# Kernel tuning notes

Measured on AMD Instinct MI355X. Metric: run time of the kernel, lower is better.

Reference implementation:

```python
import jax, jax.numpy as jnp
import numpy as np


def setup_inputs() -> dict:
    key = jax.random.key(0)
    ks = jax.random.split(key, 12)
    Tq, Tk, B, H = 1024, 1024, 8, 1024
    inp = {
        "inputs_q": jax.random.normal(ks[0], (Tq, B, H), jnp.float32),
        "inputs_kv": jax.random.normal(ks[1], (Tk, B, H), jnp.float32),
        "w_q": jax.random.normal(ks[2], (H, H), jnp.float32) * 0.02,
        "b_q": jnp.zeros((H,), jnp.float32),
        "w_kv": jax.random.normal(ks[3], (2 * H, H), jnp.float32) * 0.02,
        "b_kv": jnp.zeros((2 * H,), jnp.float32),
        "w_o": jax.random.normal(ks[4], (H, H), jnp.float32) * 0.02,
        "b_o": jnp.zeros((H,), jnp.float32),
        # BatchEnsemble rank-1 factors, initialized near 1
        "r_q": 1.0 + 0.05 * jax.random.normal(ks[5], (B, H), jnp.float32),
        "s_q": 1.0 + 0.05 * jax.random.normal(ks[6], (B, H), jnp.float32),
        "r_kv": 1.0 + 0.05 * jax.random.normal(ks[7], (B, H), jnp.float32),
        "s_kv": 1.0 + 0.05 * jax.random.normal(ks[8], (B, 2 * H), jnp.float32),
        "heads": 16,
    }
    return inp


def be_linear(x, w, b, r, s):
    # x: [T,B,Hin], w: [Hout,Hin], r: [B,Hin], s: [B,Hout]
    return jnp.einsum('tbh,oh->tbo', x * r, w) * s + b


def reference(inputs_q, inputs_kv, w_q, b_q, w_kv, b_kv, w_o, b_o,
              r_q, s_q, r_kv, s_kv, heads):
    Tq, B, H = inputs_q.shape
    Tk = inputs_kv.shape[0]
    hd = H // heads
    scale = hd ** -0.5

    q = be_linear(inputs_q, w_q, b_q, r_q, s_q)          # [Tq,B,H]
    kv = be_linear(inputs_kv, w_kv, b_kv, r_kv, s_kv)    # [Tk,B,2H]

    queries = q.reshape(Tq, B * heads, hd)
    kv = kv.reshape(Tk, B * heads, 2, hd)                # layout: head x {k,v} x hd
    keys = kv[:, :, 0, :]
    values = kv[:, :, 1, :]

    scores = jnp.einsum('qnd,knd->nqk', queries, keys) * scale  # [B*heads,Tq,Tk]
    probs = jax.nn.softmax(scores.astype(jnp.float32), axis=-1).astype(scores.dtype)
    # dropout_prob = 0 / eval: dropout is identity
    ctx = jnp.einsum('nqk,knd->qnd', probs, values).reshape(Tq, B, H)
    out = jnp.einsum('tbh,oh->tbo', ctx, w_o) + b_o      # [Tq,B,H]
    return out
```

## Files before the change

kernel.cpp:

```cpp
#include <hip/hip_runtime.h>
#include <stdint.h>

typedef unsigned short u16;
typedef __bf16 bf16x8 __attribute__((ext_vector_type(8)));
typedef float f32x4 __attribute__((ext_vector_type(4)));

typedef __attribute__((address_space(3))) void lds_void;
typedef const __attribute__((address_space(1))) void gbl_void;
#define GLD_LDS16(g, l) __builtin_amdgcn_global_load_lds((gbl_void*)(g), (lds_void*)(l), 16, 0, 0)

__device__ __forceinline__ u16 f2bf(float f) {
  unsigned u = __float_as_uint(f);
  u += 0x7fffu + ((u >> 16) & 1u);
  return (u16)(u >> 16);
}

__device__ __forceinline__ unsigned pk2bf(float a, float b) {
  unsigned au = __float_as_uint(a) + 0x8000u;
  unsigned bu = __float_as_uint(b) + 0x8000u;
  return __builtin_amdgcn_perm(bu, au, 0x07060302u);
}

__global__ void k_convert_all(const float* __restrict__ inq, const float* __restrict__ r_q,
                              const float* __restrict__ inkv, const float* __restrict__ r_kv,
                              const float* __restrict__ w_q, const float* __restrict__ w_kv,
                              const float* __restrict__ w_o,
                              u16* __restrict__ Xq, u16* __restrict__ Xkv,
                              u16* __restrict__ Wq, u16* __restrict__ Wkv,
                              u16* __restrict__ Wo) {
  int blk = blockIdx.x;
  const float* src; const float* r = nullptr; u16* dst; int base;
  if (blk < 8192)       { src = inq;  r = r_q;  dst = Xq;  base = 0; }
  else if (blk < 16384) { src = inkv; r = r_kv; dst = Xkv; base = 8192; }
  else if (blk < 17408) { src = w_q;  dst = Wq;  base = 16384; }
  else if (blk < 19456) { src = w_kv; dst = Wkv; base = 17408; }
  else                  { src = w_o;  dst = Wo;  base = 19456; }
  int i4 = ((blk - base) * 256 + threadIdx.x) * 4;
  float4 xv = *(const float4*)(src + i4);
  if (r) {
    int rb = ((i4 >> 10) & 7) * 1024 + (i4 & 1023);
    float4 rv = *(const float4*)(r + rb);
    xv.x *= rv.x; xv.y *= rv.y; xv.z *= rv.z; xv.w *= rv.w;
  }
  unsigned long long pk = (unsigned long long)pk2bf(xv.x, xv.y)
      | ((unsigned long long)pk2bf(xv.z, xv.w) << 32);
  *(unsigned long long*)(dst + i4) = pk;
}

template <int MODE>
__device__ __forceinline__ void gemm_tile(const u16* __restrict__ A, const u16* __restrict__ B,
                                          void* __restrict__ Cout, const float* __restrict__ s,
                                          const float* __restrict__ bias, int N, int K,
                                          float postscale, int bx, int by,
                                          u16* As, u16* Bs, int tid) {
  const int w = tid >> 6, lane = tid & 63;
  const int quad = lane >> 4, l16 = lane & 15;
  const int n0 = bx * 128, m0 = by * 128;
  const int wm = (w & 1) * 64, wn = (w >> 1) * 64;

  f32x4 acc[4][4] = {};

  int srow[2], scol[2];
#pragma unroll
  for (int i = 0; i < 2; ++i) {
    int p = (w * 2 + i) * 64 + lane;
    int row = p >> 2;
    int cb = (p & 3) ^ ((row >> 1) & 3);
    srow[i] = row; scol[i] = cb * 8;
  }
  int offA[4], offB[4];
#pragma unroll
  for (int t = 0; t < 4; ++t) {
    int ra = wm + t * 16 + l16;
    offA[t] = ra * 32 + ((quad ^ ((ra >> 1) & 3)) * 8);
    int rb = wn + t * 16 + l16;
    offB[t] = rb * 32 + ((quad ^ ((rb >> 1) & 3)) * 8);
  }

#pragma unroll
  for (int i = 0; i < 2; ++i) {
    GLD_LDS16(A + (size_t)(m0 + srow[i]) * K + scol[i], As + (w * 2 + i) * 512);
    GLD_LDS16(B + (size_t)(n0 + srow[i]) * K + scol[i], Bs + (w * 2 + i) * 512);
  }

  for (int k0 = 0; k0 < K; k0 += 32) {
    const int cur = (k0 >> 5) & 1;
    __syncthreads();
    if (k0 + 32 < K) {
#pragma unroll
      for (int i = 0; i < 2; ++i) {
        GLD_LDS16(A + (size_t)(m0 + srow[i]) * K + (k0 + 32) + scol[i],
                  As + (cur ^ 1) * 4096 + (w * 2 + i) * 512);
        GLD_LDS16(B + (size_t)(n0 + srow[i]) * K + (k0 + 32) + scol[i],
                  Bs + (cur ^ 1) * 4096 + (w * 2 + i) * 512);
      }
    }
    const u16* Ac = As + cur * 4096;
    const u16* Bc = Bs + cur * 4096;
    bf16x8 af[4], bfr[4];
#pragma unroll
    for (int mt = 0; mt < 4; ++mt) af[mt] = *(const bf16x8*)(Ac + offA[mt]);
#pragma unroll
    for (int nt = 0; nt < 4; ++nt) bfr[nt] = *(const bf16x8*)(Bc + offB[nt]);
#pragma unroll
    for (int mt = 0; mt < 4; ++mt)
#pragma unroll
      for (int nt = 0; nt < 4; ++nt)
        acc[mt][nt] = __builtin_amdgcn_mfma_f32_16x16x32_bf16(af[mt], bfr[nt], acc[mt][nt], 0, 0, 0);
  }

#pragma unroll
  for (int mt = 0; mt < 4; ++mt)
#pragma unroll
    for (int nt = 0; nt < 4; ++nt) {
      int n = n0 + wn + nt * 16 + l16;
#pragma unroll
      for (int rg = 0; rg < 4; ++rg) {
        int m = m0 + wm + mt * 16 + quad * 4 + rg;
        float v = acc[mt][nt][rg];
        if (MODE == 0) {
          v = (v * s[(m & 7) * N + n] + bias[n]) * postscale;
          ((u16*)Cout)[(size_t)m * N + n] = f2bf(v);
        } else {
          ((float*)Cout)[(size_t)m * N + n] = v + bias[n];
        }
      }
    }
}

__global__ void k_gemm_qkv(const u16* __restrict__ Xq, const u16* __restrict__ Wq,
                           u16* __restrict__ qout, const float* __restrict__ s_q,
                           const float* __restrict__ b_q, float qscale,
                           const u16* __restrict__ Xkv, const u16* __restrict__ Wkv,
                           u16* __restrict__ kvout, const float* __restrict__ s_kv,
                           const float* __restrict__ b_kv) {
  __shared__ __align__(16) u16 As[2 * 4096];
  __shared__ __align__(16) u16 Bs[2 * 4096];
  const int blk = blockIdx.x;
  const int xcd = blk & 7;
  const int slot = blk >> 3;
  const int bx = slot % 24;
  const int by = xcd * 8 + slot / 24;
  if (bx < 8)
    gemm_tile<0>(Xq, Wq, qout, s_q, b_q, 1024, 1024, qscale, bx, by, As, Bs, threadIdx.x);
  else
    gemm_tile<0>(Xkv, Wkv, kvout, s_kv, b_kv, 2048, 1024, 1.0f, bx - 8, by, As, Bs, threadIdx.x);
}

__global__ void k_gemm_o(const u16* __restrict__ A, const u16* __restrict__ B,
                         float* __restrict__ Cout, const float* __restrict__ bias) {
  __shared__ __align__(16) u16 As[2 * 4096];
  __shared__ __align__(16) u16 Bs[2 * 4096];
  const int blk = blockIdx.x;
  const int xcd = blk & 7;
  const int slot = blk >> 3;
  const int bx = slot % 8;
  const int by = xcd * 8 + slot / 8;
  gemm_tile<1>(A, B, Cout, nullptr, bias, 1024, 1024, 1.0f, bx, by, As, Bs, threadIdx.x);
}

__global__ void k_transpose_v(const u16* __restrict__ kv, u16* __restrict__ vt) {
  __shared__ __align__(16) u16 tile[64][72];
  const int tid = threadIdx.x;
  const int n = blockIdx.x >> 4;
  const int t0 = (blockIdx.x & 15) << 6;
#pragma unroll
  for (int it = 0; it < 2; ++it) {
    int r = it * 32 + (tid >> 3);
    int c = (tid & 7) << 3;
    *(uint4*)&tile[r][c] = *(const uint4*)(kv + ((size_t)(t0 + r) * 128 + n) * 128 + 64 + c);
  }
  __syncthreads();
#pragma unroll
  for (int it = 0; it < 2; ++it) {
    int d = it * 32 + (tid >> 3);
    int tc = (tid & 7) << 3;
    u16 v[8];
#pragma unroll
    for (int j = 0; j < 8; ++j) v[j] = tile[tc + j][d];
    uint4 o;
    o.x = (unsigned)v[0] | ((unsigned)v[1] << 16);
    o.y = (unsigned)v[2] | ((unsigned)v[3] << 16);
    o.z = (unsigned)v[4] | ((unsigned)v[5] << 16);
    o.w = (unsigned)v[6] | ((unsigned)v[7] << 16);
    *(uint4*)(vt + ((size_t)n * 64 + d) * 1024 + t0 + tc) = o;
  }
}

__global__ __launch_bounds__(256, 3) void k_attn(const u16* __restrict__ qb,
                                                 const u16* __restrict__ kvb,
                                                 const u16* __restrict__ vtb,
                                                 u16* __restrict__ ctx) {
  __shared__ __align__(16) u16 Ks[2][4096];
  __shared__ __align__(16) u16 Vts[2][4096];
  __shared__ __align__(16) u16 Ps[4][32 * 72];

  const int tid = threadIdx.x;
  const int w = tid >> 6, lane = tid & 63;
  const int quad = lane >> 4, l16 = lane & 15;
  const int n = blockIdx.x & 127;
  const int q0 = (blockIdx.x >> 7) << 7;
  const int qw = q0 + w * 32;

  bf16x8 bq[2][2];
#pragma unroll
  for (int g = 0; g < 2; ++g)
#pragma unroll
    for (int ks = 0; ks < 2; ++ks)
      bq[g][ks] = *(const bf16x8*)(qb + ((size_t)(qw + g * 16 + l16) * 128 + n) * 64 + ks * 32 + quad * 8);

  const bool isK = (w < 2);
  const int wv = w & 1;
  const u16* gbase[4];
  u16* lbase[4];
#pragma unroll
  for (int i = 0; i < 4; ++i) {
    int p = (wv * 4 + i) * 64 + lane;
    int r = p >> 3;
    int scb = ((p & 7) ^ (r & 7)) * 8;
    if (isK) {
      gbase[i] = kvb + ((size_t)r * 128 + n) * 128 + scb;
      lbase[i] = &Ks[0][(wv * 4 + i) * 512];
    } else {
      gbase[i] = vtb + ((size_t)n * 64 + r) * 1024 + scb;
      lbase[i] = &Vts[0][(wv * 4 + i) * 512];
    }
  }
  const size_t gstep = isK ? 16384 : 1;
  const int lstep = 4096;

  float l_i[2] = {0.f, 0.f};
  f32x4 accO[2][4] = {};
  u16* myP = Ps[w];

#pragma unroll
  for (int i = 0; i < 4; ++i) GLD_LDS16(gbase[i], lbase[i]);

#pragma unroll 1
  for (int tk0 = 0; tk0 < 1024; tk0 += 64) {
    const int cur = (tk0 >> 6) & 1;
    __syncthreads();
    if (tk0 < 960) {
      size_t goff = (size_t)(tk0 + 64) * gstep;
#pragma unroll
      for (int i = 0; i < 4; ++i)
        GLD_LDS16(gbase[i] + goff, lbase[i] + (cur ^ 1) * lstep);
    }
    const u16* Kc = Ks[cur];
    const u16* Vc = Vts[cur];

    f32x4 accS[2][4] = {};
#pragma unroll
    for (int mt = 0; mt < 4; ++mt) {
      int r = mt * 16 + l16;
#pragma unroll
      for (int ks = 0; ks < 2; ++ks) {
        bf16x8 ak = *(const bf16x8*)(Kc + r * 64 + (((ks * 4 + quad) ^ (r & 7)) << 3));
#pragma unroll
        for (int g = 0; g < 2; ++g)
          accS[g][mt] = __builtin_amdgcn_mfma_f32_16x16x32_bf16(ak, bq[g][ks], accS[g][mt], 0, 0, 0);
      }
    }

#pragma unroll
    for (int g = 0; g < 2; ++g) {
      float pv[16];
      float ss = 0.f;
#pragma unroll
      for (int mt = 0; mt < 4; ++mt)
#pragma unroll
        for (int rg = 0; rg < 4; ++rg) {
          float p = __builtin_amdgcn_exp2f(accS[g][mt][rg]);
          pv[mt * 4 + rg] = p;
          ss += p;
        }
      ss += __shfl_xor(ss, 16);
      ss += __shfl_xor(ss, 32);
      l_i[g] += ss;
      const int prow = (g * 16 + l16) * 72;
#pragma unroll
      for (int mt = 0; mt < 4; ++mt) {
        unsigned long long pk = (unsigned long long)pk2bf(pv[mt * 4 + 0], pv[mt * 4 + 1])
            | ((unsigned long long)pk2bf(pv[mt * 4 + 2], pv[mt * 4 + 3]) << 32);
        *(unsigned long long*)(myP + prow + mt * 16 + quad * 4) = pk;
      }
    }

    bf16x8 bp[2][2];
#pragma unroll
    for (int g = 0; g < 2; ++g)
#pragma unroll
      for (int ks = 0; ks < 2; ++ks)
        bp[g][ks] = *(const bf16x8*)(myP + (g * 16 + l16) * 72 + ks * 32 + quad * 8);
#pragma unroll
    for (int dt = 0; dt < 4; ++dt) {
      int r = dt * 16 + l16;
#pragma unroll
      for (int ks = 0; ks < 2; ++ks) {
        bf16x8 av = *(const bf16x8*)(Vc + r * 64 + (((ks * 4 + quad) ^ (r & 7)) << 3));
#pragma unroll
        for (int g = 0; g < 2; ++g)
          accO[g][dt] = __builtin_amdgcn_mfma_f32_16x16x32_bf16(av, bp[g][ks], accO[g][dt], 0, 0, 0);
      }
    }
  }

#pragma unroll
  for (int g = 0; g < 2; ++g) {
    float inv = 1.f / l_i[g];
    const size_t obase = ((size_t)(qw + g * 16 + l16) * 128 + n) * 64;
#pragma unroll
    for (int dt = 0; dt < 4; ++dt) {
      unsigned long long pk = (unsigned long long)pk2bf(accO[g][dt][0] * inv, accO[g][dt][1] * inv)
          | ((unsigned long long)pk2bf(accO[g][dt][2] * inv, accO[g][dt][3] * inv) << 32);
      *(unsigned long long*)(ctx + obase + dt * 16 + quad * 4) = pk;
    }
  }
}

extern "C" void kernel_launch(void* const* d_in, const int* in_sizes, int n_in,
                              void* d_out, int out_size, void* d_ws, size_t ws_size,
                              hipStream_t stream) {
  const float* inq  = (const float*)d_in[0];
  const float* inkv = (const float*)d_in[1];
  const float* w_q  = (const float*)d_in[2];
  const float* b_q  = (const float*)d_in[3];
  const float* w_kv = (const float*)d_in[4];
  const float* b_kv = (const float*)d_in[5];
  const float* w_o  = (const float*)d_in[6];
  const float* b_o  = (const float*)d_in[7];
  const float* r_q  = (const float*)d_in[8];
  const float* s_q  = (const float*)d_in[9];
  const float* r_kv = (const float*)d_in[10];
  const float* s_kv = (const float*)d_in[11];

  const size_t MEG = 1024 * 1024;
  u16* ws    = (u16*)d_ws;
  u16* Xq    = ws;
  u16* Xkv   = ws + 8 * MEG;
  u16* Wq    = ws + 16 * MEG;
  u16* Wkv   = ws + 17 * MEG;
  u16* Wo    = ws + 19 * MEG;
  u16* qbuf  = ws + 20 * MEG;
  u16* kvbuf = ws + 28 * MEG;
  u16* vt    = Xkv;
  u16* ctx   = Xq;

  k_convert_all<<<20480, 256, 0, stream>>>(inq, r_q, inkv, r_kv, w_q, w_kv, w_o,
                                           Xq, Xkv, Wq, Wkv, Wo);

  const float QSCALE = 0.125f * 1.44269504088896340736f;
  k_gemm_qkv<<<1536, 256, 0, stream>>>(Xq, Wq, qbuf, s_q, b_q, QSCALE,
                                       Xkv, Wkv, kvbuf, s_kv, b_kv);
  k_transpose_v<<<2048, 256, 0, stream>>>(kvbuf, vt);
  k_attn<<<1024, 256, 0, stream>>>(qbuf, kvbuf, vt, ctx);
  k_gemm_o<<<512, 256, 0, stream>>>(ctx, Wo, (float*)d_out, b_o);
}
```

Before: 296.9 us.

## Fuse V transpose into KV GEMM epilogue and triple-buffer GEMM K-loop

Removes the separate V-transpose kernel. The KV projection epilogue now writes K into a compact K buffer and V directly in transposed layout, and attention reads K with the new stride. Separately, the GEMM main loop moves from double to triple buffering with a partial vmcnt wait before each barrier, so two tiles stay in flight. The transposed V stores are strided 2-byte scatters, which may cost bandwidth, and the larger LDS footprint can lower occupancy.

After: 295.1 us. Within noise of the previous version (-0.6%).

```diff
diff --git a/kernel.cpp b/kernel.cpp
--- a/kernel.cpp
+++ b/kernel.cpp
@@ -8,6 +8,9 @@
 typedef __attribute__((address_space(3))) void lds_void;
 typedef const __attribute__((address_space(1))) void gbl_void;
 #define GLD_LDS16(g, l) __builtin_amdgcn_global_load_lds((gbl_void*)(g), (lds_void*)(l), 16, 0, 0)
+
+#define BAR_RELAX() asm volatile("s_waitcnt vmcnt(4)\n\ts_barrier" ::: "memory")
+#define BAR_FULL()  asm volatile("s_waitcnt vmcnt(0)\n\ts_barrier" ::: "memory")
 
 __device__ __forceinline__ u16 f2bf(float f) {
   unsigned u = __float_as_uint(f);
@@ -52,7 +55,8 @@
                                           void* __restrict__ Cout, const float* __restrict__ s,
                                           const float* __restrict__ bias, int N, int K,
                                           float postscale, int bx, int by,
-                                          u16* As, u16* Bs, int tid) {
+                                          u16* As, u16* Bs, int tid,
+                                          u16* __restrict__ vt, int h) {
   const int w = tid >> 6, lane = tid & 63;
   const int quad = lane >> 4, l16 = lane & 15;
   const int n0 = bx * 128, m0 = by * 128;
@@ -78,21 +82,27 @@
   }
 
 #pragma unroll
-  for (int i = 0; i < 2; ++i) {
-    GLD_LDS16(A + (size_t)(m0 + srow[i]) * K + scol[i], As + (w * 2 + i) * 512);
-    GLD_LDS16(B + (size_t)(n0 + srow[i]) * K + scol[i], Bs + (w * 2 + i) * 512);
-  }
-
+  for (int st = 0; st < 2; ++st)
+#pragma unroll
+    for (int i = 0; i < 2; ++i) {
+      GLD_LDS16(A + (size_t)(m0 + srow[i]) * K + st * 32 + scol[i],
+                As + st * 4096 + (w * 2 + i) * 512);
+      GLD_LDS16(B + (size_t)(n0 + srow[i]) * K + st * 32 + scol[i],
+                Bs + st * 4096 + (w * 2 + i) * 512);
+    }
+
+  int cur = 0, nxt = 2;
+#pragma unroll 1
   for (int k0 = 0; k0 < K; k0 += 32) {
-    const int cur = (k0 >> 5) & 1;
-    __syncthreads();
-    if (k0 + 32 < K) {
+    if (k0 + 32 >= K) BAR_FULL(); else BAR_RELAX();
+
+    if (k0 + 64 < K) {
 #pragma unroll
       for (int i = 0; i < 2; ++i) {
-        GLD_LDS16(A + (size_t)(m0 + srow[i]) * K + (k0 + 32) + scol[i],
-                  As + (cur ^ 1) * 4096 + (w * 2 + i) * 512);
-        GLD_LDS16(B + (size_t)(n0 + srow[i]) * K + (k0 + 32) + scol[i],
-                  Bs + (cur ^ 1) * 4096 + (w * 2 + i) * 512);
+        GLD_LDS16(A + (size_t)(m0 + srow[i]) * K + (k0 + 64) + scol[i],
+                  As + nxt * 4096 + (w * 2 + i) * 512);
+        GLD_LDS16(B + (size_t)(n0 + srow[i]) * K + (k0 + 64) + scol[i],
+                  Bs + nxt * 4096 + (w * 2 + i) * 512);
       }
     }
     const u16* Ac = As + cur * 4096;
@@ -107,6 +117,8 @@
 #pragma unroll
       for (int nt = 0; nt < 4; ++nt)
         acc[mt][nt] = __builtin_amdgcn_mfma_f32_16x16x32_bf16(af[mt], bfr[nt], acc[mt][nt], 0, 0, 0);
+    cur = (cur == 2) ? 0 : cur + 1;
+    nxt = (nxt == 2) ? 0 : nxt + 1;
   }
 
 #pragma unroll
@@ -121,8 +133,18 @@
         if (MODE == 0) {
           v = (v * s[(m & 7) * N + n] + bias[n]) * postscale;
           ((u16*)Cout)[(size_t)m * N + n] = f2bf(v);
+        } else if (MODE == 1) {
+          ((float*)Cout)[(size_t)m * N + n] = v + bias[n];
         } else {
-          ((float*)Cout)[(size_t)m * N + n] = v + bias[n];
+          v = v * s[(m & 7) * N + n] + bias[n];
+          int b = m & 7, tk = m >> 3;
+          int head = b * 16 + h;
+          int dloc = nt * 16 + l16;
+          if (wn == 0) {
+            ((u16*)Cout)[((size_t)(tk * 128 + head)) * 64 + dloc] = f2bf(v);
+          } else {
+            vt[((size_t)(head * 64 + dloc)) * 1024 + tk] = f2bf(v);
+          }
         }
       }
     }
@@ -132,63 +154,38 @@
                            u16* __restrict__ qout, const float* __restrict__ s_q,
                            const float* __restrict__ b_q, float qscale,
                            const u16* __restrict__ Xkv, const u16* __restrict__ Wkv,
-                           u16* __restrict__ kvout, const float* __restrict__ s_kv,
-                           const float* __restrict__ b_kv) {
-  __shared__ __align__(16) u16 As[2 * 4096];
-  __shared__ __align__(16) u16 Bs[2 * 4096];
+                           u16* __restrict__ kbuf, const float* __restrict__ s_kv,
+                           const float* __restrict__ b_kv, u16* __restrict__ vt) {
+  __shared__ __align__(16) u16 As[3 * 4096];
+  __shared__ __align__(16) u16 Bs[3 * 4096];
   const int blk = blockIdx.x;
   const int xcd = blk & 7;
   const int slot = blk >> 3;
   const int bx = slot % 24;
   const int by = xcd * 8 + slot / 24;
   if (bx < 8)
-    gemm_tile<0>(Xq, Wq, qout, s_q, b_q, 1024, 1024, qscale, bx, by, As, Bs, threadIdx.x);
+    gemm_tile<0>(Xq, Wq, qout, s_q, b_q, 1024, 1024, qscale, bx, by, As, Bs,
+                 threadIdx.x, nullptr, 0);
   else
-    gemm_tile<0>(Xkv, Wkv, kvout, s_kv, b_kv, 2048, 1024, 1.0f, bx - 8, by, As, Bs, threadIdx.x);
+    gemm_tile<2>(Xkv, Wkv, kbuf, s_kv, b_kv, 2048, 1024, 1.0f, bx - 8, by, As, Bs,
+                 threadIdx.x, vt, bx - 8);
 }
 
 __global__ void k_gemm_o(const u16* __restrict__ A, const u16* __restrict__ B,
                          float* __restrict__ Cout, const float* __restrict__ bias) {
-  __shared__ __align__(16) u16 As[2 * 4096];
-  __shared__ __align__(16) u16 Bs[2 * 4096];
+  __shared__ __align__(16) u16 As[3 * 4096];
+  __shared__ __align__(16) u16 Bs[3 * 4096];
   const int blk = blockIdx.x;
   const int xcd = blk & 7;
   const int slot = blk >> 3;
   const int bx = slot % 8;
   const int by = xcd * 8 + slot / 8;
-  gemm_tile<1>(A, B, Cout, nullptr, bias, 1024, 1024, 1.0f, bx, by, As, Bs, threadIdx.x);
-}
-
-__global__ void k_transpose_v(const u16* __restrict__ kv, u16* __restrict__ vt) {
-  __shared__ __align__(16) u16 tile[64][72];
-  const int tid = threadIdx.x;
-  const int n = blockIdx.x >> 4;
-  const int t0 = (blockIdx.x & 15) << 6;
-#pragma unroll
-  for (int it = 0; it < 2; ++it) {
-    int r = it * 32 + (tid >> 3);
-    int c = (tid & 7) << 3;
-    *(uint4*)&tile[r][c] = *(const uint4*)(kv + ((size_t)(t0 + r) * 128 + n) * 128 + 64 + c);
-  }
-  __syncthreads();
-#pragma unroll
-  for (int it = 0; it < 2; ++it) {
-    int d = it * 32 + (tid >> 3);
-    int tc = (tid & 7) << 3;
-    u16 v[8];
-#pragma unroll
-    for (int j = 0; j < 8; ++j) v[j] = tile[tc + j][d];
-    uint4 o;
-    o.x = (unsigned)v[0] | ((unsigned)v[1] << 16);
-    o.y = (unsigned)v[2] | ((unsigned)v[3] << 16);
-    o.z = (unsigned)v[4] | ((unsigned)v[5] << 16);
-    o.w = (unsigned)v[6] | ((unsigned)v[7] << 16);
-    *(uint4*)(vt + ((size_t)n * 64 + d) * 1024 + t0 + tc) = o;
-  }
+  gemm_tile<1>(A, B, Cout, nullptr, bias, 1024, 1024, 1.0f, bx, by, As, Bs,
+               threadIdx.x, nullptr, 0);
 }
 
 __global__ __launch_bounds__(256, 3) void k_attn(const u16* __restrict__ qb,
-                                                 const u16* __restrict__ kvb,
+                                                 const u16* __restrict__ kb,
                                                  const u16* __restrict__ vtb,
                                                  u16* __restrict__ ctx) {
   __shared__ __align__(16) u16 Ks[2][4096];
@@ -219,14 +216,14 @@
     int r = p >> 3;
     int scb = ((p & 7) ^ (r & 7)) * 8;
     if (isK) {
-      gbase[i] = kvb + ((size_t)r * 128 + n) * 128 + scb;
+      gbase[i] = kb + ((size_t)r * 128 + n) * 64 + scb;
       lbase[i] = &Ks[0][(wv * 4 + i) * 512];
     } else {
       gbase[i] = vtb + ((size_t)n * 64 + r) * 1024 + scb;
       lbase[i] = &Vts[0][(wv * 4 + i) * 512];
     }
   }
-  const size_t gstep = isK ? 16384 : 1;
+  const size_t gstep = isK ? 8192 : 1;
   const int lstep = 4096;
 
   float l_i[2] = {0.f, 0.f};
@@ -342,8 +339,8 @@
   u16* Wkv   = ws + 17 * MEG;
   u16* Wo    = ws + 19 * MEG;
   u16* qbuf  = ws + 20 * MEG;
-  u16* kvbuf = ws + 28 * MEG;
-  u16* vt    = Xkv;
+  u16* kbuf  = ws + 28 * MEG;
+  u16* vt    = ws + 36 * MEG;
   u16* ctx   = Xq;
 
   k_convert_all<<<20480, 256, 0, stream>>>(inq, r_q, inkv, r_kv, w_q, w_kv, w_o,
@@ -351,8 +348,7 @@
 
   const float QSCALE = 0.125f * 1.44269504088896340736f;
   k_gemm_qkv<<<1536, 256, 0, stream>>>(Xq, Wq, qbuf, s_q, b_q, QSCALE,
-                                       Xkv, Wkv, kvbuf, s_kv, b_kv);
-  k_transpose_v<<<2048, 256, 0, stream>>>(kvbuf, vt);
-  k_attn<<<1024, 256, 0, stream>>>(qbuf, kvbuf, vt, ctx);
+                                       Xkv, Wkv, kbuf, s_kv, b_kv, vt);
+  k_attn<<<1024, 256, 0, stream>>>(qbuf, kbuf, vt, ctx);
   k_gemm_o<<<512, 256, 0, stream>>>(ctx, Wo, (float*)d_out, b_o);
 }
```
